# Performance work log

Measured on AMD Instinct MI355X. Metric: run time of the kernel, lower is better.

The kernel has to match this reference:

```python
import jax, jax.numpy as jnp
import numpy as np

N, D = 512, 256          # n candidates, span_emb_size
R = 4                    # num relation types / etypes
FF = 512                 # mention_linker_ffnn_size, depth 1
L = 2                    # ieg_bignn_hidden_layers
DH = D // 2              # GraphConvolution output size


def setup_inputs() -> dict:
    key = jax.random.key(0)
    ks = jax.random.split(key, 12)
    s = lambda fan_in: 1.0 / np.sqrt(fan_in)
    return {
        "candidate_embs": jax.random.normal(ks[0], (N, D), jnp.float32),
        # relation scorer FFNN: 3D -> FF -> R
        "W_sc0": jax.random.normal(ks[1], (3 * D, FF), jnp.float32) * s(3 * D),
        "b_sc0": jnp.zeros((FF,), jnp.float32),
        "W_sc1": jax.random.normal(ks[2], (FF, R), jnp.float32) * s(FF),
        "b_sc1": jnp.zeros((R,), jnp.float32),
        # BiGCN: per-layer, per-relation fw/bw GraphConvolution D -> D//2
        "W_fw": jax.random.normal(ks[3], (L, R, D, DH), jnp.float32) * s(D),
        "b_fw": jnp.zeros((L, R, DH), jnp.float32),
        "W_bw": jax.random.normal(ks[4], (L, R, D, DH), jnp.float32) * s(D),
        "b_bw": jnp.zeros((L, R, DH), jnp.float32),
        # per-layer linear1: D -> D
        "W_lin": jax.random.normal(ks[5], (L, D, D), jnp.float32) * s(D),
        "b_lin": jnp.zeros((L, D), jnp.float32),
    }


def reference(candidate_embs, W_sc0, b_sc0, W_sc1, b_sc1,
              W_fw, b_fw, W_bw, b_bw, W_lin, b_lin):
    n, d = candidate_embs.shape
    # --- get_pair_embs: [n, n, 3d] = cat(src, target, src*target) ---
    src = jnp.broadcast_to(candidate_embs[None, :, :], (n, n, d))   # row i varies j
    tgt = jnp.broadcast_to(candidate_embs[:, None, :], (n, n, d))
    pair = jnp.concatenate([src, tgt, src * tgt], axis=-1)          # [n, n, 3d]
    # --- relation scorer FFNN (ReLU hidden, dropout=0 at inference) ---
    h = jax.nn.relu(jnp.einsum('ijk,kf->ijf', pair, W_sc0) + b_sc0)
    scores = jnp.einsum('ijf,fr->ijr', h, W_sc1) + b_sc1            # [n, n, R]
    probs = jax.nn.softmax(scores, axis=-1)
    # --- adjs_from_preds: detach, zero diagonal; bw = fw^T ---
    probs = jax.lax.stop_gradient(probs)
    A = jnp.moveaxis(probs, -1, 0)                                   # [R, n, n]
    eye = jnp.eye(n, dtype=bool)
    A = jnp.where(eye[None, :, :], 0.0, A)
    AT = jnp.swapaxes(A, 1, 2)
    # --- BiGCN: L layers of multi-relation bi-directional GCN ---
    x = candidate_embs
    for l in range(L):
        sup_fw = jnp.einsum('nd,rde->rne', x, W_fw[l])               # [R, n, DH]
        sup_bw = jnp.einsum('nd,rde->rne', x, W_bw[l])
        fw = jnp.einsum('rij,rje->rie', A, sup_fw) + b_fw[l][:, None, :]
        bw = jnp.einsum('rij,rje->rie', AT, sup_bw) + b_bw[l][:, None, :]
        outs = jnp.concatenate([bw, fw], axis=-1)                    # [R, n, D]
        x = jax.nn.relu(outs.sum(axis=0)) @ W_lin[l] + b_lin[l] + x  # residual
    return x
```

## Files before the change

### kernel.cpp

```cpp
#include <hip/hip_runtime.h>
#include <hip/hip_bf16.h>

using f32x4  = __attribute__((ext_vector_type(4))) float;
using bf16x8 = __attribute__((ext_vector_type(8))) short;

__device__ __forceinline__ unsigned short f2bf(float f) {
    union { __hip_bfloat16 h; unsigned short u; } cv;
    cv.h = __float2bfloat16(f);
    return cv.u;
}
__device__ __forceinline__ unsigned int pack2bf(float lo, float hi) {
    float2 t; t.x = lo; t.y = hi;
    union { __hip_bfloat162 h; unsigned int u; } cv;
    cv.h = __float22bfloat162_rn(t);
    return cv.u;
}
__device__ __forceinline__ float bf2f(unsigned short u) {
    return __uint_as_float((unsigned)u << 16);
}

__global__ __launch_bounds__(512) void prep_kernel(
        const float* __restrict__ E, const float* __restrict__ Wsc0, const float* __restrict__ Wsc1,
        const float* __restrict__ Wfw, const float* __restrict__ bfw,
        const float* __restrict__ Wbw, const float* __restrict__ bbw,
        const float* __restrict__ Wlin,
        unsigned short* __restrict__ E16, unsigned short* __restrict__ W0p,
        unsigned short* __restrict__ WabP,
        unsigned short* __restrict__ WcatT, unsigned short* __restrict__ WlinT,
        float* __restrict__ bsumS, unsigned short* __restrict__ W1p) {
    const int NE = 131072, NW0 = 131072, NWAB = 262144, NCAT = 524288, NLIN = 131072, NW1P = 8192;
    const int total = NE + NW0 + NWAB + NCAT + NLIN + NW1P + 512;
    for (int idx = blockIdx.x * 512 + threadIdx.x; idx < total; idx += 512 * 512) {
        int t = idx;
        if (t < NE) { E16[t] = f2bf(E[t]); continue; }
        t -= NE;
        if (t < NW0) {
            int e = t & 7, lane = (t >> 3) & 63, kk = (t >> 9) & 7, nb = (t >> 12) & 3, w = (t >> 14) & 7;
            int fcol = w * 64 + nb * 16 + (lane & 15);
            int k = kk * 32 + (lane >> 4) * 8 + e;
            W0p[t] = f2bf(Wsc0[(512 + k) * 512 + fcol]);
            continue;
        }
        t -= NW0;
        if (t < NWAB) {
            int e = t & 7, lane = (t >> 3) & 63, kk = (t >> 9) & 7, nb = (t >> 12) & 3, wf = t >> 14;
            int fcol = wf * 64 + nb * 16 + (lane & 15);
            int k = kk * 32 + (lane >> 4) * 8 + e;
            int row = (fcol < 512) ? k : (256 + k);
            WabP[t] = f2bf(Wsc0[row * 512 + (fcol & 511)]);
            continue;
        }
        t -= NWAB;
        if (t < NCAT) {
            int e = t & 127, k = (t >> 7) & 255, r = (t >> 15) & 3, d = (t >> 17) & 1, l = t >> 18;
            const float* src = (d == 0) ? Wfw : Wbw;
            float v = src[((l * 4 + r) * 256 + k) * 128 + e];
            WcatT[(l * 1024 + d * 512 + r * 128 + e) * 256 + k] = f2bf(v);
            continue;
        }
        t -= NCAT;
        if (t < NLIN) {
            int d = t & 255, f = (t >> 8) & 255, l = t >> 16;
            WlinT[(l * 256 + d) * 256 + f] = f2bf(Wlin[(l * 256 + f) * 256 + d]);
            continue;
        }
        t -= NLIN;
        if (t < NW1P) {
            int e = t & 7, lane = (t >> 3) & 63, kap = t >> 9;
            int fp = kap * 32 + (lane >> 4) * 8 + e;
            int w = fp >> 6, q = (fp >> 2) & 15, nb = fp & 3;
            int f = w * 64 + nb * 16 + q;
            int r = lane & 15;
            W1p[t] = (r < 4) ? f2bf(Wsc1[f * 4 + r]) : (unsigned short)0;
            continue;
        }
        t -= NW1P;
        {
            int f = t & 255, l = t >> 8;
            float s = 0.f;
            if (f < 128) { for (int r = 0; r < 4; ++r) s += bbw[(l * 4 + r) * 128 + f]; }
            else         { for (int r = 0; r < 4; ++r) s += bfw[(l * 4 + r) * 128 + (f - 128)]; }
            bsumS[l * 256 + f] = s;
        }
    }
}

__global__ __launch_bounds__(512) void uv_kernel(const unsigned short* __restrict__ E16,
                                                 const unsigned short* __restrict__ WabP,
                                                 const float* __restrict__ bsc0,
                                                 unsigned short* __restrict__ Upk,
                                                 unsigned short* __restrict__ VT16) {
    __shared__ unsigned short sE[32 * 256];
    const int jt = blockIdx.x;
    const int tid = threadIdx.x, lane = tid & 63, w = tid >> 6;
    const int l15 = lane & 15, l4 = lane >> 4;
#pragma unroll
    for (int it = 0; it < 2; ++it) {
        int u = it * 512 + tid;
        int row = u >> 5, slot = u & 31;
        uint4 v = *(const uint4*)(E16 + (jt * 32 + row) * 256 + slot * 8);
        *(uint4*)((char*)sE + row * 512 + ((slot * 16) ^ ((row & 7) << 4))) = v;
    }
    __syncthreads();
    const bf16x8* Wab8 = (const bf16x8*)WabP;
    f32x4 acc[2][8];
#pragma unroll
    for (int a_ = 0; a_ < 2; ++a_)
#pragma unroll
        for (int b_ = 0; b_ < 8; ++b_) acc[a_][b_] = (f32x4){0.f, 0.f, 0.f, 0.f};
#pragma unroll
    for (int kk = 0; kk < 8; ++kk) {
        bf16x8 af[2];
#pragma unroll
        for (int mbl = 0; mbl < 2; ++mbl) {
            int row = mbl * 16 + l15;
            af[mbl] = *(const bf16x8*)((char*)sE + row * 512 + ((kk * 64 + l4 * 16) ^ ((row & 7) << 4)));
        }
#pragma unroll
        for (int nb = 0; nb < 8; ++nb) {
            int wf = 2 * w + (nb >> 2);
            bf16x8 bfr = Wab8[((wf * 4 + (nb & 3)) * 8 + kk) * 64 + lane];
#pragma unroll
            for (int mbl = 0; mbl < 2; ++mbl)
                acc[mbl][nb] = __builtin_amdgcn_mfma_f32_16x16x32_bf16(af[mbl], bfr, acc[mbl][nb], 0, 0, 0);
        }
    }
#pragma unroll
    for (int mbl = 0; mbl < 2; ++mbl) {
        int j_base = jt * 32 + mbl * 16 + l4 * 4;
#pragma unroll
        for (int nb = 0; nb < 8; ++nb) {
            int f_g = (2 * w + (nb >> 2)) * 64 + (nb & 3) * 16 + l15;
            ushort4 o;
            if (f_g < 512) {
                float b0f = bsc0[f_g];
                o.x = f2bf(acc[mbl][nb][0] + b0f);
                o.y = f2bf(acc[mbl][nb][1] + b0f);
                o.z = f2bf(acc[mbl][nb][2] + b0f);
                o.w = f2bf(acc[mbl][nb][3] + b0f);
                int idx = (((j_base >> 6) * 8 + (f_g >> 6)) * 4 + ((j_base >> 4) & 3)) * 4 + ((f_g >> 4) & 3);
                *(ushort4*)(Upk + (idx * 64 + (l4 * 16 + l15)) * 4) = o;
            } else {
                o.x = f2bf(acc[mbl][nb][0]);
                o.y = f2bf(acc[mbl][nb][1]);
                o.z = f2bf(acc[mbl][nb][2]);
                o.w = f2bf(acc[mbl][nb][3]);
                *(ushort4*)(VT16 + (f_g - 512) * 512 + j_base) = o;
            }
        }
    }
}

__global__ __launch_bounds__(512) void pair_kernel(
    const float* __restrict__ E, const unsigned short* __restrict__ W0p,
    const unsigned short* __restrict__ Upk, const unsigned short* __restrict__ VT16,
    const unsigned short* __restrict__ W1p, const float* __restrict__ b1,
    unsigned short* __restrict__ A16) {

    __shared__ unsigned short prodL[64 * 256];
    __shared__ float scoresL[64 * 4];

    const int i = blockIdx.x;
    const int jt = blockIdx.y;
    const int j0 = jt * 64;
    const int tid = threadIdx.x;
    const int lane = tid & 63;
    const int w = tid >> 6;
    const int l15 = lane & 15, l4 = lane >> 4;

    float Vv[4];
#pragma unroll
    for (int nb = 0; nb < 4; ++nb) Vv[nb] = bf2f(VT16[(w * 64 + nb * 16 + l15) * 512 + i]);
    f32x4 acc[4][4];
#pragma unroll
    for (int mb = 0; mb < 4; ++mb)
#pragma unroll
        for (int nb = 0; nb < 4; ++nb) {
            int idx4 = (((jt * 8 + w) * 4 + mb) * 4 + nb) * 64 + lane;
            ushort4 uq = ((const ushort4*)Upk)[idx4];
            acc[mb][nb][0] = bf2f(uq.x) + Vv[nb];
            acc[mb][nb][1] = bf2f(uq.y) + Vv[nb];
            acc[mb][nb][2] = bf2f(uq.z) + Vv[nb];
            acc[mb][nb][3] = bf2f(uq.w) + Vv[nb];
        }

    {
        int m = tid >> 3;
        const float4* ej = (const float4*)(E + (j0 + m) * 256);
        const float4* ei = (const float4*)(E + i * 256);
        char* base = (char*)prodL;
#pragma unroll
        for (int c = 0; c < 8; ++c) {
            int q = (tid & 7) + c * 8;
            float4 a = ej[q], b = ei[q];
            uint2 val;
            val.x = pack2bf(a.x * b.x, a.y * b.y);
            val.y = pack2bf(a.z * b.z, a.w * b.w);
            int byteoff = m * 512 + ((q * 8) ^ ((m & 7) << 4));
            *(uint2*)(base + byteoff) = val;
        }
    }
    __syncthreads();

    const char* pbase = (const char*)prodL;
    const bf16x8* Wp8 = (const bf16x8*)W0p;
#pragma unroll
    for (int kk = 0; kk < 8; ++kk) {
        bf16x8 afr[4], bfr[4];
#pragma unroll
        for (int mb = 0; mb < 4; ++mb) {
            int row = mb * 16 + l15;
            int off = row * 512 + ((kk * 64 + l4 * 16) ^ ((row & 7) << 4));
            afr[mb] = *(const bf16x8*)(pbase + off);
        }
#pragma unroll
        for (int nb = 0; nb < 4; ++nb)
            bfr[nb] = Wp8[((w * 4 + nb) * 8 + kk) * 64 + lane];
#pragma unroll
        for (int mb = 0; mb < 4; ++mb)
#pragma unroll
            for (int nb = 0; nb < 4; ++nb)
                acc[mb][nb] = __builtin_amdgcn_mfma_f32_16x16x32_bf16(afr[mb], bfr[nb], acc[mb][nb], 0, 0, 0);
    }

    if (tid < 256) scoresL[tid] = b1[tid & 3];
    __syncthreads();

    char* hb = (char*)prodL;
    const bf16x8* W1p8 = (const bf16x8*)W1p;
    bf16x8 w1f[2];
#pragma unroll
    for (int kl = 0; kl < 2; ++kl) w1f[kl] = W1p8[(w * 2 + kl) * 64 + lane];

    f32x4 accS[4];
#pragma unroll
    for (int q = 0; q < 4; ++q) accS[q] = (f32x4){0.f, 0.f, 0.f, 0.f};

#pragma unroll
    for (int p = 0; p < 2; ++p) {
#pragma unroll
        for (int mbl = 0; mbl < 2; ++mbl) {
            int mb = p * 2 + mbl;
#pragma unroll
            for (int reg = 0; reg < 4; ++reg) {
                int rl = mbl * 16 + l4 * 4 + reg;
                float h0 = fmaxf(acc[mb][0][reg], 0.f);
                float h1 = fmaxf(acc[mb][1][reg], 0.f);
                float h2 = fmaxf(acc[mb][2][reg], 0.f);
                float h3 = fmaxf(acc[mb][3][reg], 0.f);
                uint2 val;
                val.x = pack2bf(h0, h1);
                val.y = pack2bf(h2, h3);
                *(uint2*)(hb + rl * 1024 + ((w * 128 + l15 * 8) ^ ((rl & 7) << 4))) = val;
            }
        }
        __syncthreads();
#pragma unroll
        for (int mbl = 0; mbl < 2; ++mbl) {
            int rl = mbl * 16 + l15;
#pragma unroll
            for (int kl = 0; kl < 2; ++kl) {
                bf16x8 ha = *(const bf16x8*)(hb + rl * 1024 + (((w * 2 + kl) * 64 + l4 * 16) ^ ((rl & 7) << 4)));
                accS[p * 2 + mbl] = __builtin_amdgcn_mfma_f32_16x16x32_bf16(ha, w1f[kl], accS[p * 2 + mbl], 0, 0, 0);
            }
        }
        __syncthreads();
    }

    if (l15 < 4) {
#pragma unroll
        for (int q = 0; q < 4; ++q)
#pragma unroll
            for (int reg = 0; reg < 4; ++reg)
                atomicAdd(&scoresL[(q * 16 + l4 * 4 + reg) * 4 + l15], accS[q][reg]);
    }
    __syncthreads();
    if (tid < 64) {
        int m = tid, j = j0 + m;
        float s0 = scoresL[m * 4 + 0], s1 = scoresL[m * 4 + 1];
        float sA = scoresL[m * 4 + 2], sB = scoresL[m * 4 + 3];
        float mx = fmaxf(fmaxf(s0, s1), fmaxf(sA, sB));
        float e0 = __expf(s0 - mx), e1 = __expf(s1 - mx), e2 = __expf(sA - mx), e3 = __expf(sB - mx);
        float inv = 1.f / (e0 + e1 + e2 + e3);
        float p_[4] = {e0 * inv, e1 * inv, e2 * inv, e3 * inv};
        if (j == i) { p_[0] = p_[1] = p_[2] = p_[3] = 0.f; }
#pragma unroll
        for (int r = 0; r < 4; ++r)
            A16[(r * 512 + i) * 512 + j] = f2bf(p_[r]);
    }
}

template<int K>
__device__ __forceinline__ void stageP(unsigned short* lds, const unsigned short* g, int ldg, int tid) {
    constexpr int SLOTS = K / 8;
#pragma unroll
    for (int it = 0; it < (32 * SLOTS) / 256; ++it) {
        int u = it * 256 + tid;
        int row = u / SLOTS, slot = u % SLOTS;
        uint4 v = *(const uint4*)(g + row * ldg + slot * 8);
        *(uint4*)((char*)lds + row * (K * 2) + ((slot * 16) ^ ((row & 7) << 4))) = v;
    }
}
__device__ __forceinline__ void stage64(unsigned short* lds, const unsigned short* g, int ldg, int tid) {
#pragma unroll
    for (int it = 0; it < 8; ++it) {
        int u = it * 256 + tid;
        int row = u >> 5, slot = u & 31;
        uint4 v = *(const uint4*)(g + row * ldg + slot * 8);
        *(uint4*)((char*)lds + row * 512 + ((slot * 16) ^ ((row & 7) << 4))) = v;
    }
}
template<int K>
__device__ __forceinline__ bf16x8 fragP(const unsigned short* lds, int row, int kc, int l4) {
    return *(const bf16x8*)((const char*)lds + row * (K * 2) + ((((kc * 4 + l4) * 16) ^ ((row & 7) << 4))));
}

__global__ __launch_bounds__(256) void c1_kernel(const unsigned short* __restrict__ WcatT,
                                                 const unsigned short* __restrict__ x16,
                                                 unsigned short* __restrict__ supT,
                                                 const unsigned short* __restrict__ A16,
                                                 unsigned short* __restrict__ AT16, int l) {
    __shared__ unsigned short lA[32 * 256], lB[32 * 256];
    int tid = threadIdx.x;
    if (blockIdx.y >= 16) {
        auto t = (unsigned short(*)[65])lA;
        int job = (blockIdx.y - 16) * 32 + blockIdx.x;
        int r = job >> 6, ty = (job >> 3) & 7, tx = job & 7;
        const unsigned short* src = A16 + (r * 512 + ty * 64) * 512 + tx * 64;
        unsigned short* dst = AT16 + (r * 512 + tx * 64) * 512 + ty * 64;
#pragma unroll
        for (int it = 0; it < 2; ++it) {
            int u = it * 256 + tid, row = u >> 3, c8 = (u & 7) * 8;
            uint4 v = *(const uint4*)(src + row * 512 + c8);
            const unsigned short* p = (const unsigned short*)&v;
#pragma unroll
            for (int e = 0; e < 8; ++e) t[c8 + e][row] = p[e];
        }
        __syncthreads();
#pragma unroll
        for (int it = 0; it < 2; ++it) {
            int u = it * 256 + tid, row = u >> 3, c8 = (u & 7) * 8;
            uint4 v; unsigned short* p = (unsigned short*)&v;
#pragma unroll
            for (int e = 0; e < 8; ++e) p[e] = t[row][c8 + e];
            *(uint4*)(dst + row * 512 + c8) = v;
        }
        return;
    }
    int c0 = blockIdx.x * 32, jt0 = blockIdx.y * 32;
    int lane = tid & 63, w = tid >> 6;
    int wr = (w >> 1) * 16, wc = (w & 1) * 16;
    int l15 = lane & 15, l4 = lane >> 4;
    stageP<256>(lA, WcatT + l * 262144 + c0 * 256, 256, tid);
    stageP<256>(lB, x16 + jt0 * 256, 256, tid);
    __syncthreads();
    f32x4 a0 = {0.f,0.f,0.f,0.f}, a1 = {0.f,0.f,0.f,0.f};
#pragma unroll
    for (int kc = 0; kc < 8; kc += 2) {
        a0 = __builtin_amdgcn_mfma_f32_16x16x32_bf16(fragP<256>(lA, wr + l15, kc, l4),
                                                     fragP<256>(lB, wc + l15, kc, l4), a0, 0, 0, 0);
        a1 = __builtin_amdgcn_mfma_f32_16x16x32_bf16(fragP<256>(lA, wr + l15, kc + 1, l4),
                                                     fragP<256>(lB, wc + l15, kc + 1, l4), a1, 0, 0, 0);
    }
    f32x4 acc = a0 + a1;
#pragma unroll
    for (int reg = 0; reg < 4; ++reg) {
        int c = c0 + wr + l4 * 4 + reg;
        int j = jt0 + wc + l15;
        supT[c * 512 + j] = f2bf(acc[reg]);
    }
}

__global__ __launch_bounds__(256) void c2_kernel(const unsigned short* __restrict__ A16,
                                                 const unsigned short* __restrict__ AT16,
                                                 const unsigned short* __restrict__ supT,
                                                 float* __restrict__ Pc2) {
    __shared__ unsigned short lA[64 * 256], lB[64 * 256];
    int i0 = blockIdx.x * 64, f0 = blockIdx.y * 64;
    int s = blockIdx.z, r = s >> 1, kh = s & 1;
    bool bw = (f0 < 128);
    int e0 = bw ? f0 : (f0 - 128);
    const unsigned short* Am = bw ? AT16 : A16;
    int tid = threadIdx.x, lane = tid & 63, w = tid >> 6;
    int wr = (w >> 1) * 32, wc = (w & 1) * 32;
    int l15 = lane & 15, l4 = lane >> 4;
    stage64(lA, Am + (r * 512 + i0) * 512 + kh * 256, 512, tid);
    stage64(lB, supT + ((bw ? 512 : 0) + r * 128 + e0) * 512 + kh * 256, 512, tid);
    __syncthreads();
    f32x4 acc[2][2];
#pragma unroll
    for (int a_ = 0; a_ < 2; ++a_)
#pragma unroll
        for (int b_ = 0; b_ < 2; ++b_) acc[a_][b_] = (f32x4){0.f, 0.f, 0.f, 0.f};
#pragma unroll
    for (int kc = 0; kc < 8; ++kc) {
        bf16x8 af[2], bf_[2];
#pragma unroll
        for (int mb = 0; mb < 2; ++mb) af[mb] = fragP<256>(lA, wr + mb * 16 + l15, kc, l4);
#pragma unroll
        for (int nb = 0; nb < 2; ++nb) bf_[nb] = fragP<256>(lB, wc + nb * 16 + l15, kc, l4);
#pragma unroll
        for (int mb = 0; mb < 2; ++mb)
#pragma unroll
            for (int nb = 0; nb < 2; ++nb)
                acc[mb][nb] = __builtin_amdgcn_mfma_f32_16x16x32_bf16(af[mb], bf_[nb], acc[mb][nb], 0, 0, 0);
    }
    float* dst = Pc2 + s * 131072;
#pragma unroll
    for (int mb = 0; mb < 2; ++mb)
#pragma unroll
        for (int nb = 0; nb < 2; ++nb)
#pragma unroll
            for (int reg = 0; reg < 4; ++reg)
                dst[(i0 + wr + mb * 16 + l4 * 4 + reg) * 256 + f0 + wc + nb * 16 + l15] = acc[mb][nb][reg];
}

__global__ __launch_bounds__(256) void c3_kernel(const float* __restrict__ Pc2,
                                                 const float* __restrict__ bsumS,
                                                 const unsigned short* __restrict__ WlinT,
                                                 const float* __restrict__ blin,
                                                 const float* __restrict__ xold,
                                                 float* __restrict__ xnew,
                                                 unsigned short* __restrict__ x16out, int l) {
    __shared__ unsigned short lA[32 * 256], lB[32 * 256];
    int i0 = blockIdx.x * 32, d0 = blockIdx.y * 32;
    int tid = threadIdx.x, lane = tid & 63, w = tid >> 6;
    int wr = (w >> 1) * 16, wc = (w & 1) * 16;
    int l15 = lane & 15, l4 = lane >> 4;
#pragma unroll
    for (int g = 0; g < 4; ++g) {
        int u = g * 256 + tid;
        int row = u >> 5, k8 = (u & 31) * 8;
        float s[8] = {0,0,0,0,0,0,0,0};
#pragma unroll
        for (int s8 = 0; s8 < 8; ++s8) {
            const float4* p = (const float4*)(Pc2 + s8 * 131072 + (i0 + row) * 256 + k8);
            float4 a = p[0], b = p[1];
            s[0] += a.x; s[1] += a.y; s[2] += a.z; s[3] += a.w;
            s[4] += b.x; s[5] += b.y; s[6] += b.z; s[7] += b.w;
        }
        uint4 v;
        unsigned* vp = (unsigned*)&v;
#pragma unroll
        for (int e2 = 0; e2 < 4; ++e2) {
            float lo = fmaxf(s[e2 * 2] + bsumS[l * 256 + k8 + e2 * 2], 0.f);
            float hi = fmaxf(s[e2 * 2 + 1] + bsumS[l * 256 + k8 + e2 * 2 + 1], 0.f);
            vp[e2] = pack2bf(lo, hi);
        }
        *(uint4*)((char*)lA + row * 512 + ((k8 * 2) ^ ((row & 7) << 4))) = v;
    }
    stageP<256>(lB, WlinT + l * 65536 + d0 * 256, 256, tid);
    __syncthreads();
    f32x4 a0 = {0.f,0.f,0.f,0.f}, a1 = {0.f,0.f,0.f,0.f};
#pragma unroll
    for (int kc = 0; kc < 8; kc += 2) {
        a0 = __builtin_amdgcn_mfma_f32_16x16x32_bf16(fragP<256>(lA, wr + l15, kc, l4),
                                                     fragP<256>(lB, wc + l15, kc, l4), a0, 0, 0, 0);
        a1 = __builtin_amdgcn_mfma_f32_16x16x32_bf16(fragP<256>(lA, wr + l15, kc + 1, l4),
                                                     fragP<256>(lB, wc + l15, kc + 1, l4), a1, 0, 0, 0);
    }
    f32x4 acc = a0 + a1;
#pragma unroll
    for (int reg = 0; reg < 4; ++reg) {
        int ii = i0 + wr + l4 * 4 + reg;
        int dd = d0 + wc + l15;
        float vv = acc[reg] + blin[l * 256 + dd] + xold[ii * 256 + dd];
        xnew[ii * 256 + dd] = vv;
        x16out[ii * 256 + dd] = f2bf(vv);
    }
}

extern "C" void kernel_launch(void* const* d_in, const int* in_sizes, int n_in,
                              void* d_out, int out_size, void* d_ws, size_t ws_size,
                              hipStream_t stream) {
    const float* E    = (const float*)d_in[0];
    const float* Wsc0 = (const float*)d_in[1];
    const float* bsc0 = (const float*)d_in[2];
    const float* Wsc1 = (const float*)d_in[3];
    const float* bsc1 = (const float*)d_in[4];
    const float* Wfw  = (const float*)d_in[5];
    const float* bfw  = (const float*)d_in[6];
    const float* Wbw  = (const float*)d_in[7];
    const float* bbw  = (const float*)d_in[8];
    const float* Wlin = (const float*)d_in[9];
    const float* blin = (const float*)d_in[10];
    float* out = (float*)d_out;

    char* ws = (char*)d_ws;
    size_t off = 0;
    unsigned short* E16   = (unsigned short*)(ws + off); off += 512 * 256 * 2;
    unsigned short* W0p   = (unsigned short*)(ws + off); off += 512 * 256 * 2;
    unsigned short* WabP  = (unsigned short*)(ws + off); off += 1024 * 256 * 2;
    unsigned short* WcatT = (unsigned short*)(ws + off); off += 2 * 1024 * 256 * 2;
    unsigned short* WlinT = (unsigned short*)(ws + off); off += 2 * 256 * 256 * 2;
    float* bsumS          = (float*)(ws + off);          off += 2 * 256 * 4;
    unsigned short* Upk   = (unsigned short*)(ws + off); off += 512 * 512 * 2;
    unsigned short* VT16  = (unsigned short*)(ws + off); off += 512 * 512 * 2;
    unsigned short* W1p   = (unsigned short*)(ws + off); off += 16 * 64 * 8 * 2;
    unsigned short* A16   = (unsigned short*)(ws + off); off += 4 * 512 * 512 * 2;
    unsigned short* AT16  = (unsigned short*)(ws + off); off += 4 * 512 * 512 * 2;
    unsigned short* supT  = (unsigned short*)(ws + off); off += 1024 * 512 * 2;
    float* Pc2            = (float*)(ws + off);          off += 8 * 512 * 256 * 4;
    float* xf1            = (float*)(ws + off);          off += 512 * 256 * 4;
    unsigned short* x16_1 = (unsigned short*)(ws + off); off += 512 * 256 * 2;

    prep_kernel<<<512, 512, 0, stream>>>(E, Wsc0, Wsc1, Wfw, bfw, Wbw, bbw, Wlin,
                                         E16, W0p, WabP, WcatT, WlinT, bsumS, W1p);
    uv_kernel<<<16, 512, 0, stream>>>(E16, WabP, bsc0, Upk, VT16);
    pair_kernel<<<dim3(512, 8), 512, 0, stream>>>(E, W0p, Upk, VT16, W1p, bsc1, A16);

    for (int l = 0; l < 2; ++l) {
        const unsigned short* xin16 = (l == 0) ? E16 : x16_1;
        const float* xoldf = (l == 0) ? E : xf1;
        float* xout = (l == 0) ? xf1 : out;
        c1_kernel<<<dim3(32, (l == 0) ? 24 : 16), 256, 0, stream>>>(WcatT, xin16, supT, A16, AT16, l);
        c2_kernel<<<dim3(8, 4, 8), 256, 0, stream>>>(A16, AT16, supT, Pc2);
        c3_kernel<<<dim3(16, 8), 256, 0, stream>>>(Pc2, bsumS, WlinT, blin, xoldf, xout, x16_1, l);
    }
    (void)in_sizes; (void)n_in; (void)out_size; (void)ws_size;
}
```

Before: 199.6 us.

## Process two source rows per pair_kernel block to reuse W0 fragments

```diff
diff --git a/kernel.cpp b/kernel.cpp
--- a/kernel.cpp
+++ b/kernel.cpp
@@ -89,7 +89,7 @@
                                                  const unsigned short* __restrict__ WabP,
                                                  const float* __restrict__ bsc0,
                                                  unsigned short* __restrict__ Upk,
-                                                 unsigned short* __restrict__ VT16) {
+                                                 float* __restrict__ V) {
     __shared__ unsigned short sE[32 * 256];
     const int jt = blockIdx.x;
     const int tid = threadIdx.x, lane = tid & 63, w = tid >> 6;
@@ -129,38 +129,40 @@
     for (int mbl = 0; mbl < 2; ++mbl) {
         int j_base = jt * 32 + mbl * 16 + l4 * 4;
 #pragma unroll
-        for (int nb = 0; nb < 8; ++nb) {
-            int f_g = (2 * w + (nb >> 2)) * 64 + (nb & 3) * 16 + l15;
-            ushort4 o;
+        for (int nb8 = 0; nb8 < 8; ++nb8) {
+            int f_g = (2 * w + (nb8 >> 2)) * 64 + (nb8 & 3) * 16 + l15;
             if (f_g < 512) {
                 float b0f = bsc0[f_g];
-                o.x = f2bf(acc[mbl][nb][0] + b0f);
-                o.y = f2bf(acc[mbl][nb][1] + b0f);
-                o.z = f2bf(acc[mbl][nb][2] + b0f);
-                o.w = f2bf(acc[mbl][nb][3] + b0f);
-                int idx = (((j_base >> 6) * 8 + (f_g >> 6)) * 4 + ((j_base >> 4) & 3)) * 4 + ((f_g >> 4) & 3);
-                *(ushort4*)(Upk + (idx * 64 + (l4 * 16 + l15)) * 4) = o;
+                ushort4 o;
+                o.x = f2bf(acc[mbl][nb8][0] + b0f);
+                o.y = f2bf(acc[mbl][nb8][1] + b0f);
+                o.z = f2bf(acc[mbl][nb8][2] + b0f);
+                o.w = f2bf(acc[mbl][nb8][3] + b0f);
+                int jtp = j_base >> 6, mbp = (j_base >> 4) & 3;
+                int wp = f_g >> 6, nbp = (f_g >> 4) & 3;
+                int lanep = l4 * 16 + l15;
+                *(ushort4*)(Upk + ((((jtp * 8 + wp) * 4 + mbp) * 2 + (nbp >> 1)) * 64 + lanep) * 8 + (nbp & 1) * 4) = o;
             } else {
-                o.x = f2bf(acc[mbl][nb][0]);
-                o.y = f2bf(acc[mbl][nb][1]);
-                o.z = f2bf(acc[mbl][nb][2]);
-                o.w = f2bf(acc[mbl][nb][3]);
-                *(ushort4*)(VT16 + (f_g - 512) * 512 + j_base) = o;
+                int fv = f_g - 512;
+#pragma unroll
+                for (int reg = 0; reg < 4; ++reg)
+                    V[(j_base + reg) * 512 + fv] = acc[mbl][nb8][reg];
             }
         }
     }
 }
 
-__global__ __launch_bounds__(512) void pair_kernel(
-    const float* __restrict__ E, const unsigned short* __restrict__ W0p,
-    const unsigned short* __restrict__ Upk, const unsigned short* __restrict__ VT16,
+__global__ __launch_bounds__(512, 2) void pair_kernel(
+    const unsigned short* __restrict__ E16, const unsigned short* __restrict__ W0p,
+    const unsigned short* __restrict__ Upk, const float* __restrict__ V,
     const unsigned short* __restrict__ W1p, const float* __restrict__ b1,
     unsigned short* __restrict__ A16) {
 
-    __shared__ unsigned short prodL[64 * 256];
-    __shared__ float scoresL[64 * 4];
-
-    const int i = blockIdx.x;
+    __shared__ unsigned short bufL[2 * 64 * 256];
+    __shared__ float vrow[2][512];
+    __shared__ float scoresL[2][256];
+
+    const int i0 = blockIdx.x * 2, i1 = i0 + 1;
     const int jt = blockIdx.y;
     const int j0 = jt * 64;
     const int tid = threadIdx.x;
@@ -168,125 +170,147 @@
     const int w = tid >> 6;
     const int l15 = lane & 15, l4 = lane >> 4;
 
-    float Vv[4];
-#pragma unroll
-    for (int nb = 0; nb < 4; ++nb) Vv[nb] = bf2f(VT16[(w * 64 + nb * 16 + l15) * 512 + i]);
-    f32x4 acc[4][4];
-#pragma unroll
-    for (int mb = 0; mb < 4; ++mb)
-#pragma unroll
-        for (int nb = 0; nb < 4; ++nb) {
-            int idx4 = (((jt * 8 + w) * 4 + mb) * 4 + nb) * 64 + lane;
-            ushort4 uq = ((const ushort4*)Upk)[idx4];
-            acc[mb][nb][0] = bf2f(uq.x) + Vv[nb];
-            acc[mb][nb][1] = bf2f(uq.y) + Vv[nb];
-            acc[mb][nb][2] = bf2f(uq.z) + Vv[nb];
-            acc[mb][nb][3] = bf2f(uq.w) + Vv[nb];
-        }
+    vrow[0][tid] = V[i0 * 512 + tid];
+    vrow[1][tid] = V[i1 * 512 + tid];
+    if (tid < 256) { scoresL[0][tid] = b1[tid & 3]; scoresL[1][tid] = b1[tid & 3]; }
 
     {
         int m = tid >> 3;
-        const float4* ej = (const float4*)(E + (j0 + m) * 256);
-        const float4* ei = (const float4*)(E + i * 256);
-        char* base = (char*)prodL;
-#pragma unroll
-        for (int c = 0; c < 8; ++c) {
-            int q = (tid & 7) + c * 8;
-            float4 a = ej[q], b = ei[q];
-            uint2 val;
-            val.x = pack2bf(a.x * b.x, a.y * b.y);
-            val.y = pack2bf(a.z * b.z, a.w * b.w);
-            int byteoff = m * 512 + ((q * 8) ^ ((m & 7) << 4));
-            *(uint2*)(base + byteoff) = val;
-        }
-    }
+        int slot = tid & 7;
+        const bf16x8* ejp  = (const bf16x8*)(E16 + (j0 + m) * 256 + slot * 32);
+        const bf16x8* ei0p = (const bf16x8*)(E16 + i0 * 256 + slot * 32);
+        const bf16x8* ei1p = (const bf16x8*)(E16 + i1 * 256 + slot * 32);
+        char* base = (char*)bufL;
+#pragma unroll
+        for (int c = 0; c < 4; ++c) {
+            bf16x8 ej = ejp[c], e0 = ei0p[c], e1 = ei1p[c];
+            uint4 v0, v1;
+            unsigned* p0 = (unsigned*)&v0;
+            unsigned* p1 = (unsigned*)&v1;
+#pragma unroll
+            for (int e2 = 0; e2 < 4; ++e2) {
+                float jl = bf2f((unsigned short)ej[e2 * 2]), jh = bf2f((unsigned short)ej[e2 * 2 + 1]);
+                p0[e2] = pack2bf(jl * bf2f((unsigned short)e0[e2 * 2]), jh * bf2f((unsigned short)e0[e2 * 2 + 1]));
+                p1[e2] = pack2bf(jl * bf2f((unsigned short)e1[e2 * 2]), jh * bf2f((unsigned short)e1[e2 * 2 + 1]));
+            }
+            int off = m * 512 + ((slot * 64 + c * 16) ^ ((m & 7) << 4));
+            *(uint4*)(base + off) = v0;
+            *(uint4*)(base + 32768 + off) = v1;
+        }
+    }
+
+    f32x4 acc0[4][4], acc1[4][4];
+#pragma unroll
+    for (int mb = 0; mb < 4; ++mb)
+#pragma unroll
+        for (int nbh = 0; nbh < 2; ++nbh) {
+            uint4 u4 = *(const uint4*)(Upk + ((((jt * 8 + w) * 4 + mb) * 2 + nbh) * 64 + lane) * 8);
+            const unsigned short* us = (const unsigned short*)&u4;
+#pragma unroll
+            for (int h = 0; h < 2; ++h) {
+                int nb = nbh * 2 + h;
+                float v0f = vrow[0][w * 64 + nb * 16 + l15];
+                float v1f = vrow[1][w * 64 + nb * 16 + l15];
+#pragma unroll
+                for (int reg = 0; reg < 4; ++reg) {
+                    float uu = bf2f(us[h * 4 + reg]);
+                    acc0[mb][nb][reg] = uu + v0f;
+                    acc1[mb][nb][reg] = uu + v1f;
+                }
+            }
+        }
     __syncthreads();
 
-    const char* pbase = (const char*)prodL;
+    const char* pbase = (const char*)bufL;
     const bf16x8* Wp8 = (const bf16x8*)W0p;
 #pragma unroll
     for (int kk = 0; kk < 8; ++kk) {
-        bf16x8 afr[4], bfr[4];
+        bf16x8 bfr[4];
+#pragma unroll
+        for (int nb = 0; nb < 4; ++nb)
+            bfr[nb] = Wp8[((w * 4 + nb) * 8 + kk) * 64 + lane];
+        bf16x8 afr[4];
 #pragma unroll
         for (int mb = 0; mb < 4; ++mb) {
             int row = mb * 16 + l15;
-            int off = row * 512 + ((kk * 64 + l4 * 16) ^ ((row & 7) << 4));
-            afr[mb] = *(const bf16x8*)(pbase + off);
-        }
-#pragma unroll
-        for (int nb = 0; nb < 4; ++nb)
-            bfr[nb] = Wp8[((w * 4 + nb) * 8 + kk) * 64 + lane];
+            afr[mb] = *(const bf16x8*)(pbase + row * 512 + ((kk * 64 + l4 * 16) ^ ((row & 7) << 4)));
+        }
 #pragma unroll
         for (int mb = 0; mb < 4; ++mb)
 #pragma unroll
             for (int nb = 0; nb < 4; ++nb)
-                acc[mb][nb] = __builtin_amdgcn_mfma_f32_16x16x32_bf16(afr[mb], bfr[nb], acc[mb][nb], 0, 0, 0);
-    }
-
-    if (tid < 256) scoresL[tid] = b1[tid & 3];
+                acc0[mb][nb] = __builtin_amdgcn_mfma_f32_16x16x32_bf16(afr[mb], bfr[nb], acc0[mb][nb], 0, 0, 0);
+#pragma unroll
+        for (int mb = 0; mb < 4; ++mb) {
+            int row = mb * 16 + l15;
+            afr[mb] = *(const bf16x8*)(pbase + 32768 + row * 512 + ((kk * 64 + l4 * 16) ^ ((row & 7) << 4)));
+        }
+#pragma unroll
+        for (int mb = 0; mb < 4; ++mb)
+#pragma unroll
+            for (int nb = 0; nb < 4; ++nb)
+                acc1[mb][nb] = __builtin_amdgcn_mfma_f32_16x16x32_bf16(afr[mb], bfr[nb], acc1[mb][nb], 0, 0, 0);
+    }
     __syncthreads();
 
-    char* hb = (char*)prodL;
+    char* hb = (char*)bufL;
     const bf16x8* W1p8 = (const bf16x8*)W1p;
     bf16x8 w1f[2];
 #pragma unroll
     for (int kl = 0; kl < 2; ++kl) w1f[kl] = W1p8[(w * 2 + kl) * 64 + lane];
 
-    f32x4 accS[4];
-#pragma unroll
-    for (int q = 0; q < 4; ++q) accS[q] = (f32x4){0.f, 0.f, 0.f, 0.f};
-
-#pragma unroll
-    for (int p = 0; p < 2; ++p) {
-#pragma unroll
-        for (int mbl = 0; mbl < 2; ++mbl) {
-            int mb = p * 2 + mbl;
+#pragma unroll
+    for (int ii = 0; ii < 2; ++ii) {
+#pragma unroll
+        for (int mb = 0; mb < 4; ++mb)
 #pragma unroll
             for (int reg = 0; reg < 4; ++reg) {
-                int rl = mbl * 16 + l4 * 4 + reg;
-                float h0 = fmaxf(acc[mb][0][reg], 0.f);
-                float h1 = fmaxf(acc[mb][1][reg], 0.f);
-                float h2 = fmaxf(acc[mb][2][reg], 0.f);
-                float h3 = fmaxf(acc[mb][3][reg], 0.f);
+                int rl = mb * 16 + l4 * 4 + reg;
+                f32x4* A = (ii == 0) ? &acc0[mb][0] : &acc1[mb][0];
+                float h0 = fmaxf(A[0][reg], 0.f);
+                float h1 = fmaxf(A[1][reg], 0.f);
+                float h2 = fmaxf(A[2][reg], 0.f);
+                float h3 = fmaxf(A[3][reg], 0.f);
                 uint2 val;
                 val.x = pack2bf(h0, h1);
                 val.y = pack2bf(h2, h3);
                 *(uint2*)(hb + rl * 1024 + ((w * 128 + l15 * 8) ^ ((rl & 7) << 4))) = val;
             }
-        }
         __syncthreads();
-#pragma unroll
-        for (int mbl = 0; mbl < 2; ++mbl) {
-            int rl = mbl * 16 + l15;
+        f32x4 accS[4];
+#pragma unroll
+        for (int mb = 0; mb < 4; ++mb) {
+            accS[mb] = (f32x4){0.f, 0.f, 0.f, 0.f};
+            int rl = mb * 16 + l15;
 #pragma unroll
             for (int kl = 0; kl < 2; ++kl) {
                 bf16x8 ha = *(const bf16x8*)(hb + rl * 1024 + (((w * 2 + kl) * 64 + l4 * 16) ^ ((rl & 7) << 4)));
-                accS[p * 2 + mbl] = __builtin_amdgcn_mfma_f32_16x16x32_bf16(ha, w1f[kl], accS[p * 2 + mbl], 0, 0, 0);
+                accS[mb] = __builtin_amdgcn_mfma_f32_16x16x32_bf16(ha, w1f[kl], accS[mb], 0, 0, 0);
             }
         }
+        if (l15 < 4) {
+#pragma unroll
+            for (int mb = 0; mb < 4; ++mb)
+#pragma unroll
+                for (int reg = 0; reg < 4; ++reg)
+                    atomicAdd(&scoresL[ii][(mb * 16 + l4 * 4 + reg) * 4 + l15], accS[mb][reg]);
+        }
         __syncthreads();
     }
 
-    if (l15 < 4) {
-#pragma unroll
-        for (int q = 0; q < 4; ++q)
-#pragma unroll
-            for (int reg = 0; reg < 4; ++reg)
-                atomicAdd(&scoresL[(q * 16 + l4 * 4 + reg) * 4 + l15], accS[q][reg]);
-    }
-    __syncthreads();
-    if (tid < 64) {
-        int m = tid, j = j0 + m;
-        float s0 = scoresL[m * 4 + 0], s1 = scoresL[m * 4 + 1];
-        float sA = scoresL[m * 4 + 2], sB = scoresL[m * 4 + 3];
+    if (tid < 128) {
+        int ii = tid >> 6, m = tid & 63;
+        int j = j0 + m, ic = i0 + ii;
+        float s0 = scoresL[ii][m * 4 + 0], s1 = scoresL[ii][m * 4 + 1];
+        float sA = scoresL[ii][m * 4 + 2], sB = scoresL[ii][m * 4 + 3];
         float mx = fmaxf(fmaxf(s0, s1), fmaxf(sA, sB));
         float e0 = __expf(s0 - mx), e1 = __expf(s1 - mx), e2 = __expf(sA - mx), e3 = __expf(sB - mx);
         float inv = 1.f / (e0 + e1 + e2 + e3);
         float p_[4] = {e0 * inv, e1 * inv, e2 * inv, e3 * inv};
-        if (j == i) { p_[0] = p_[1] = p_[2] = p_[3] = 0.f; }
+        if (j == ic) { p_[0] = p_[1] = p_[2] = p_[3] = 0.f; }
 #pragma unroll
         for (int r = 0; r < 4; ++r)
-            A16[(r * 512 + i) * 512 + j] = f2bf(p_[r]);
+            A16[(r * 512 + ic) * 512 + j] = f2bf(p_[r]);
     }
 }
 
@@ -495,7 +519,7 @@
     unsigned short* WlinT = (unsigned short*)(ws + off); off += 2 * 256 * 256 * 2;
     float* bsumS          = (float*)(ws + off);          off += 2 * 256 * 4;
     unsigned short* Upk   = (unsigned short*)(ws + off); off += 512 * 512 * 2;
-    unsigned short* VT16  = (unsigned short*)(ws + off); off += 512 * 512 * 2;
+    float* V              = (float*)(ws + off);          off += 512 * 512 * 4;
     unsigned short* W1p   = (unsigned short*)(ws + off); off += 16 * 64 * 8 * 2;
     unsigned short* A16   = (unsigned short*)(ws + off); off += 4 * 512 * 512 * 2;
     unsigned short* AT16  = (unsigned short*)(ws + off); off += 4 * 512 * 512 * 2;
@@ -506,8 +530,8 @@
 
     prep_kernel<<<512, 512, 0, stream>>>(E, Wsc0, Wsc1, Wfw, bfw, Wbw, bbw, Wlin,
                                          E16, W0p, WabP, WcatT, WlinT, bsumS, W1p);
-    uv_kernel<<<16, 512, 0, stream>>>(E16, WabP, bsc0, Upk, VT16);
-    pair_kernel<<<dim3(512, 8), 512, 0, stream>>>(E, W0p, Upk, VT16, W1p, bsc1, A16);
+    uv_kernel<<<16, 512, 0, stream>>>(E16, WabP, bsc0, Upk, V);
+    pair_kernel<<<dim3(256, 8), 512, 0, stream>>>(E16, W0p, Upk, V, W1p, bsc1, A16);
 
     for (int l = 0; l < 2; ++l) {
         const unsigned short* xin16 = (l == 0) ? E16 : x16_1;
```

Measured after the change: 187.3 us. -6.1%, faster.
